# Kernel tuning notes

Hardware: AMD Instinct MI355X
Metric: run time of the kernel (lower is better)

Reference implementation:

```python
import jax, jax.numpy as jnp
import numpy as np

N_NODES = 50000
N_EDGES = 800000
D_IN = 1024
D_OUT = 256
LEAKY_SLOPE = 0.01  # F.leaky_relu default


def setup_inputs() -> dict:
    key = jax.random.key(0)
    k_x, k_w, k_b, k_src, k_dst, k_ew, k_norm = jax.random.split(key, 7)
    x = jax.random.normal(k_x, (N_NODES, D_IN), dtype=jnp.float32)
    # xavier_uniform-style scale for the weight
    limit = np.sqrt(6.0 / (D_IN + D_OUT)).astype(np.float32)
    weight = jax.random.uniform(k_w, (D_IN, D_OUT), dtype=jnp.float32, minval=-limit, maxval=limit)
    stdv = 1.0 / np.sqrt(D_OUT)
    bias = jax.random.uniform(k_b, (D_OUT,), dtype=jnp.float32, minval=-stdv, maxval=stdv)
    src = jax.random.randint(k_src, (N_EDGES,), 0, N_NODES, dtype=jnp.int64)
    dst = jax.random.randint(k_dst, (N_EDGES,), 0, N_NODES, dtype=jnp.int64)
    edge_index = jnp.stack([src, dst], axis=0)  # [2, E]
    edge_weight = jax.random.uniform(k_ew, (N_EDGES,), dtype=jnp.float32)
    norm = jax.random.uniform(k_norm, (N_NODES, 1), dtype=jnp.float32) + 0.5  # avoid div-by-~0
    return {"x": x, "weight": weight, "bias": bias, "edge_index": edge_index,
            "edge_weight": edge_weight, "norm": norm}


def reference(x, weight, bias, edge_index, edge_weight, norm):
    # support = input @ W            [N, D_OUT]
    support = x @ weight
    src = edge_index[0]
    dst = edge_index[1]
    # spmm(adj, support): out[i] = sum_{e: dst_e == i} w_e * support[src_e]
    msgs = support[src] * edge_weight[:, None]            # [E, D_OUT]
    out = jax.ops.segment_sum(msgs, dst, num_segments=x.shape[0])  # [N, D_OUT]
    out = out / norm + bias
    return jax.nn.leaky_relu(out, negative_slope=LEAKY_SLOPE)
```

## Files before the change

### kernel.cpp

```cpp
#include <hip/hip_runtime.h>
#include <hip/hip_bf16.h>

#define N_NODES 50000
#define N_EDGES 800000
#define D_IN    1024
#define D_OUT   256
#define CAP     64
#define LEAKY   0.01f

typedef __attribute__((ext_vector_type(8))) short bf16x8;
typedef __attribute__((ext_vector_type(4))) float f32x4;
typedef __attribute__((ext_vector_type(4))) int   i32x4;
typedef unsigned short u16;

__device__ __forceinline__ u16 f2bfu(float f) {
  uint32_t x = __float_as_uint(f);
  uint32_t r = (x + 0x7FFFu + ((x >> 16) & 1u)) >> 16;
  return (u16)r;
}
__device__ __forceinline__ float bfu2f(u16 u) {
  return __uint_as_float(((uint32_t)u) << 16);
}
__device__ __forceinline__ int swz2(int b) { return b ^ (((b >> 11) & 7) << 4); }

__global__ __launch_bounds__(256) void wconv_kernel(const float* __restrict__ w,
                                                    char* __restrict__ img,
                                                    int* __restrict__ deg) {
  const int t = blockIdx.x * 256 + threadIdx.x;
  if (t < N_NODES) deg[t] = 0;
  const int t2z = t + 32768;
  if (t2z < N_NODES) deg[t2z] = 0;

  const int s   = t >> 13;
  const int r13 = t & 8191;
  const int tt  = r13 >> 8;
  const int rem = r13 & 255;
  const int i   = rem >> 6;
  const int ln  = rem & 63;
  const int n   = s * 64 + i * 16 + (ln & 15);
  const int k0  = tt * 32 + (ln >> 4) * 8;
  bf16x8 v;
#pragma unroll
  for (int j = 0; j < 8; ++j) v[j] = (short)f2bfu(w[(size_t)(k0 + j) * D_OUT + n]);
  *(bf16x8*)(img + (size_t)t * 16) = v;
}

#define BM 64
#define GEMM_BLOCKS ((N_NODES + BM - 1) / BM)
#define BUILD_BLOCKS 64

__global__ __launch_bounds__(512) void gemm_build_kernel(
    const float* __restrict__ x, const char* __restrict__ img,
    u16* __restrict__ support,
    const int* __restrict__ ei, const float* __restrict__ ew,
    int* __restrict__ deg, int2* __restrict__ csr) {
  __shared__ char Xlds[BM * 2048];

  if (blockIdx.x < BUILD_BLOCKS) {
    const int t0 = blockIdx.x * 512 + threadIdx.x;
    for (int e = t0; e < N_EDGES; e += BUILD_BLOCKS * 512) {
      const int src = ei[e];
      const int dst = ei[N_EDGES + e];
      const float w = ew[e];
      const int slot = atomicAdd(&deg[dst], 1);
      if (slot < CAP) csr[dst * CAP + slot] = make_int2(src, __float_as_int(w));
    }
    return;
  }

  const int tid  = threadIdx.x;
  const int lane = tid & 63;
  const int wid  = tid >> 6;
  const int wn   = wid & 3;
  const int wm   = wid >> 2;
  const int l15  = lane & 15;
  const int l16  = lane >> 4;
  const int m0   = (blockIdx.x - BUILD_BLOCKS) * BM;

  {
    const int row  = tid >> 3;
    const int col8 = (tid & 7) * 8;
    const int xr   = min(m0 + row, N_NODES - 1);
    const float* xp = x + (size_t)xr * D_IN + col8;
#pragma unroll
    for (int c = 0; c < 16; ++c) {
      const f32x4 a = __builtin_nontemporal_load((const f32x4*)(xp + c * 64));
      const f32x4 b = __builtin_nontemporal_load((const f32x4*)(xp + c * 64 + 4));
      bf16x8 v;
      v[0] = (short)f2bfu(a[0]); v[1] = (short)f2bfu(a[1]);
      v[2] = (short)f2bfu(a[2]); v[3] = (short)f2bfu(a[3]);
      v[4] = (short)f2bfu(b[0]); v[5] = (short)f2bfu(b[1]);
      v[6] = (short)f2bfu(b[2]); v[7] = (short)f2bfu(b[3]);
      *(bf16x8*)(Xlds + swz2(row * 2048 + c * 128 + col8 * 2)) = v;
    }
  }
  __syncthreads();

  f32x4 acc[4][2];
#pragma unroll
  for (int i = 0; i < 4; ++i)
#pragma unroll
    for (int j = 0; j < 2; ++j) acc[i][j] = (f32x4)0.0f;

  const char* wp = img + (size_t)wn * 131072 + lane * 16;
  int xoff[2];
#pragma unroll
  for (int j = 0; j < 2; ++j)
    xoff[j] = (wm * 32 + j * 16 + l15) * 2048 + l16 * 16;

  bf16x8 afA[4], afB[4], bbA[2], bbB[2];
#pragma unroll
  for (int i = 0; i < 4; ++i) afA[i] = *(const bf16x8*)(wp + i * 1024);
#pragma unroll
  for (int j = 0; j < 2; ++j) bbA[j] = *(const bf16x8*)(Xlds + swz2(xoff[j]));

  for (int t = 0; t < 32; t += 2) {
#pragma unroll
    for (int i = 0; i < 4; ++i)
      afB[i] = *(const bf16x8*)(wp + (t + 1) * 4096 + i * 1024);
#pragma unroll
    for (int j = 0; j < 2; ++j)
      bbB[j] = *(const bf16x8*)(Xlds + swz2(xoff[j] + (t + 1) * 64));
#pragma unroll
    for (int i = 0; i < 4; ++i)
#pragma unroll
      for (int j = 0; j < 2; ++j)
        acc[i][j] = __builtin_amdgcn_mfma_f32_16x16x32_bf16(afA[i], bbA[j], acc[i][j], 0, 0, 0);
    if (t < 30) {
#pragma unroll
      for (int i = 0; i < 4; ++i)
        afA[i] = *(const bf16x8*)(wp + (t + 2) * 4096 + i * 1024);
#pragma unroll
      for (int j = 0; j < 2; ++j)
        bbA[j] = *(const bf16x8*)(Xlds + swz2(xoff[j] + (t + 2) * 64));
    }
#pragma unroll
    for (int i = 0; i < 4; ++i)
#pragma unroll
      for (int j = 0; j < 2; ++j)
        acc[i][j] = __builtin_amdgcn_mfma_f32_16x16x32_bf16(afB[i], bbB[j], acc[i][j], 0, 0, 0);
  }

#pragma unroll
  for (int j = 0; j < 2; ++j) {
    const int m = m0 + wm * 32 + j * 16 + l15;
    if (m < N_NODES) {
#pragma unroll
      for (int i = 0; i < 4; ++i) {
        const int n = wn * 64 + i * 16 + l16 * 4;
        ushort4 o;
        o.x = f2bfu(acc[i][j][0]);
        o.y = f2bfu(acc[i][j][1]);
        o.z = f2bfu(acc[i][j][2]);
        o.w = f2bfu(acc[i][j][3]);
        *(ushort4*)&support[(size_t)m * D_OUT + n] = o;
      }
    }
  }
}

__global__ __launch_bounds__(256) void agg_kernel(const u16* __restrict__ support,
                                                  const int* __restrict__ deg,
                                                  const int2* __restrict__ csr,
                                                  const float* __restrict__ norm,
                                                  const float* __restrict__ bias,
                                                  float* __restrict__ out) {
  const int lane = threadIdx.x & 63;
  const int wid  = threadIdx.x >> 6;
  const int node = blockIdx.x * 4 + wid;
  const int d    = min(deg[node], CAP);
  const int cb   = node * CAP;
  const int ch   = lane * 4;

  float a0 = 0.f, a1 = 0.f, a2 = 0.f, a3 = 0.f;
  int s = 0;

  for (; s + 16 <= d; s += 16) {
    i32x4 q[8];
#pragma unroll
    for (int i = 0; i < 8; ++i)
      q[i] = __builtin_nontemporal_load((const i32x4*)&csr[cb + s + 2 * i]);
    ushort4 v[16];
#pragma unroll
    for (int i = 0; i < 8; ++i) {
      v[2 * i]     = *(const ushort4*)&support[(size_t)q[i][0] * D_OUT + ch];
      v[2 * i + 1] = *(const ushort4*)&support[(size_t)q[i][2] * D_OUT + ch];
    }
#pragma unroll
    for (int i = 0; i < 8; ++i) {
      const float wa = __int_as_float(q[i][1]);
      const float wb = __int_as_float(q[i][3]);
      a0 = fmaf(wa, bfu2f(v[2 * i].x), a0);
      a1 = fmaf(wa, bfu2f(v[2 * i].y), a1);
      a2 = fmaf(wa, bfu2f(v[2 * i].z), a2);
      a3 = fmaf(wa, bfu2f(v[2 * i].w), a3);
      a0 = fmaf(wb, bfu2f(v[2 * i + 1].x), a0);
      a1 = fmaf(wb, bfu2f(v[2 * i + 1].y), a1);
      a2 = fmaf(wb, bfu2f(v[2 * i + 1].z), a2);
      a3 = fmaf(wb, bfu2f(v[2 * i + 1].w), a3);
    }
  }

  for (; s + 8 <= d; s += 8) {
    i32x4 q[4];
#pragma unroll
    for (int i = 0; i < 4; ++i)
      q[i] = __builtin_nontemporal_load((const i32x4*)&csr[cb + s + 2 * i]);
    ushort4 v[8];
#pragma unroll
    for (int i = 0; i < 4; ++i) {
      v[2 * i]     = *(const ushort4*)&support[(size_t)q[i][0] * D_OUT + ch];
      v[2 * i + 1] = *(const ushort4*)&support[(size_t)q[i][2] * D_OUT + ch];
    }
#pragma unroll
    for (int i = 0; i < 4; ++i) {
      const float wa = __int_as_float(q[i][1]);
      const float wb = __int_as_float(q[i][3]);
      a0 = fmaf(wa, bfu2f(v[2 * i].x), a0);
      a1 = fmaf(wa, bfu2f(v[2 * i].y), a1);
      a2 = fmaf(wa, bfu2f(v[2 * i].z), a2);
      a3 = fmaf(wa, bfu2f(v[2 * i].w), a3);
      a0 = fmaf(wb, bfu2f(v[2 * i + 1].x), a0);
      a1 = fmaf(wb, bfu2f(v[2 * i + 1].y), a1);
      a2 = fmaf(wb, bfu2f(v[2 * i + 1].z), a2);
      a3 = fmaf(wb, bfu2f(v[2 * i + 1].w), a3);
    }
  }

  for (; s < d; ++s) {
    const int2  e   = csr[cb + s];
    const float wgt = __int_as_float(e.y);
    const ushort4 v = *(const ushort4*)&support[(size_t)e.x * D_OUT + ch];
    a0 = fmaf(wgt, bfu2f(v.x), a0);
    a1 = fmaf(wgt, bfu2f(v.y), a1);
    a2 = fmaf(wgt, bfu2f(v.z), a2);
    a3 = fmaf(wgt, bfu2f(v.w), a3);
  }

  const float rn = 1.0f / norm[node];
  const float4 b = *(const float4*)&bias[ch];
  float o0 = fmaf(a0, rn, b.x);
  float o1 = fmaf(a1, rn, b.y);
  float o2 = fmaf(a2, rn, b.z);
  float o3 = fmaf(a3, rn, b.w);
  o0 = o0 > 0.f ? o0 : o0 * LEAKY;
  o1 = o1 > 0.f ? o1 : o1 * LEAKY;
  o2 = o2 > 0.f ? o2 : o2 * LEAKY;
  o3 = o3 > 0.f ? o3 : o3 * LEAKY;
  f32x4 ov;
  ov[0] = o0; ov[1] = o1; ov[2] = o2; ov[3] = o3;
  __builtin_nontemporal_store(ov, (f32x4*)&out[(size_t)node * D_OUT + ch]);
}

extern "C" void kernel_launch(void* const* d_in, const int* in_sizes, int n_in,
                              void* d_out, int out_size, void* d_ws, size_t ws_size,
                              hipStream_t stream) {
  const float* x    = (const float*)d_in[0];
  const float* w    = (const float*)d_in[1];
  const float* bias = (const float*)d_in[2];
  const int*   ei   = (const int*)d_in[3];
  const float* ew   = (const float*)d_in[4];
  const float* norm = (const float*)d_in[5];
  float* out = (float*)d_out;

  char* ws = (char*)d_ws;
  u16*   support = (u16*)  (ws);
  char*  img     =         (ws + 25600000);
  int2*  csr     = (int2*) (ws + 26124288);
  int*   deg     = (int*)  (ws + 51724288);

  wconv_kernel<<<128, 256, 0, stream>>>(w, img, deg);
  gemm_build_kernel<<<BUILD_BLOCKS + GEMM_BLOCKS, 512, 0, stream>>>(
      x, img, support, ei, ew, deg, csr);
  agg_kernel<<<N_NODES / 4, 256, 0, stream>>>(support, deg, csr, norm, bias, out);
}
```

Baseline: 183.0 us.

## Drop LDS staging; load x directly into registers with larger per-wave GEMM tiles

The GEMM no longer stages a converted 64-row x tile in shared memory. Each wave now loads fp32 x rows straight from global memory into registers, converts them to bf16 in-register, and computes a 64x128 output tile with double-buffered x fragments. The weight image is re-laid out to match, and blocks shrink to 256 threads covering two M-tiles. This removes the LDS footprint and the block-wide barrier to raise occupancy and overlap loads with MFMA, at the cost of much higher register pressure and less coalesced global x loads.

```diff
diff --git a/kernel.cpp b/kernel.cpp
--- a/kernel.cpp
+++ b/kernel.cpp
@@ -21,44 +21,39 @@
 __device__ __forceinline__ float bfu2f(u16 u) {
   return __uint_as_float(((uint32_t)u) << 16);
 }
-__device__ __forceinline__ int swz2(int b) { return b ^ (((b >> 11) & 7) << 4); }
 
 __global__ __launch_bounds__(256) void wconv_kernel(const float* __restrict__ w,
-                                                    char* __restrict__ img,
+                                                    char* __restrict__ wimg,
                                                     int* __restrict__ deg) {
-  const int t = blockIdx.x * 256 + threadIdx.x;
-  if (t < N_NODES) deg[t] = 0;
-  const int t2z = t + 32768;
-  if (t2z < N_NODES) deg[t2z] = 0;
-
-  const int s   = t >> 13;
-  const int r13 = t & 8191;
-  const int tt  = r13 >> 8;
-  const int rem = r13 & 255;
-  const int i   = rem >> 6;
-  const int ln  = rem & 63;
-  const int n   = s * 64 + i * 16 + (ln & 15);
-  const int k0  = tt * 32 + (ln >> 4) * 8;
+  const int u = blockIdx.x * 256 + threadIdx.x;
+  if (u < N_NODES) deg[u] = 0;
+  const int u2 = u + 32768;
+  if (u2 < N_NODES) deg[u2] = 0;
+
+  const int lane = u & 63;
+  const int nf   = (u >> 6) & 7;
+  const int wn   = (u >> 9) & 1;
+  const int t    = u >> 10;
+  const int n    = wn * 128 + nf * 16 + (lane & 15);
+  const int k0   = t * 32 + (lane >> 4) * 8;
   bf16x8 v;
 #pragma unroll
   for (int j = 0; j < 8; ++j) v[j] = (short)f2bfu(w[(size_t)(k0 + j) * D_OUT + n]);
-  *(bf16x8*)(img + (size_t)t * 16) = v;
-}
-
-#define BM 64
-#define GEMM_BLOCKS ((N_NODES + BM - 1) / BM)
-#define BUILD_BLOCKS 64
-
-__global__ __launch_bounds__(512) void gemm_build_kernel(
-    const float* __restrict__ x, const char* __restrict__ img,
+  *(bf16x8*)(wimg + (size_t)u * 16) = v;
+}
+
+#define MT_TILES ((N_NODES + 63) / 64)
+#define GEMM_BLOCKS ((MT_TILES + 1) / 2)
+#define BUILD_BLOCKS 60
+
+__global__ __launch_bounds__(256) void gemm_build_kernel(
+    const float* __restrict__ x, const char* __restrict__ wimg,
     u16* __restrict__ support,
     const int* __restrict__ ei, const float* __restrict__ ew,
     int* __restrict__ deg, int2* __restrict__ csr) {
-  __shared__ char Xlds[BM * 2048];
-
   if (blockIdx.x < BUILD_BLOCKS) {
-    const int t0 = blockIdx.x * 512 + threadIdx.x;
-    for (int e = t0; e < N_EDGES; e += BUILD_BLOCKS * 512) {
+    const int t0 = blockIdx.x * 256 + threadIdx.x;
+    for (int e = t0; e < N_EDGES; e += BUILD_BLOCKS * 256) {
       const int src = ei[e];
       const int dst = ei[N_EDGES + e];
       const float w = ew[e];
@@ -68,91 +63,88 @@
     return;
   }
 
+  const int bi   = blockIdx.x - BUILD_BLOCKS;
   const int tid  = threadIdx.x;
   const int lane = tid & 63;
   const int wid  = tid >> 6;
-  const int wn   = wid & 3;
-  const int wm   = wid >> 2;
+  const int mt   = bi * 2 + (wid >> 1);
+  const int wn   = wid & 1;
   const int l15  = lane & 15;
   const int l16  = lane >> 4;
-  const int m0   = (blockIdx.x - BUILD_BLOCKS) * BM;
-
-  {
-    const int row  = tid >> 3;
-    const int col8 = (tid & 7) * 8;
-    const int xr   = min(m0 + row, N_NODES - 1);
-    const float* xp = x + (size_t)xr * D_IN + col8;
-#pragma unroll
-    for (int c = 0; c < 16; ++c) {
-      const f32x4 a = __builtin_nontemporal_load((const f32x4*)(xp + c * 64));
-      const f32x4 b = __builtin_nontemporal_load((const f32x4*)(xp + c * 64 + 4));
-      bf16x8 v;
-      v[0] = (short)f2bfu(a[0]); v[1] = (short)f2bfu(a[1]);
-      v[2] = (short)f2bfu(a[2]); v[3] = (short)f2bfu(a[3]);
-      v[4] = (short)f2bfu(b[0]); v[5] = (short)f2bfu(b[1]);
-      v[6] = (short)f2bfu(b[2]); v[7] = (short)f2bfu(b[3]);
-      *(bf16x8*)(Xlds + swz2(row * 2048 + c * 128 + col8 * 2)) = v;
-    }
-  }
-  __syncthreads();
-
-  f32x4 acc[4][2];
-#pragma unroll
-  for (int i = 0; i < 4; ++i)
-#pragma unroll
-    for (int j = 0; j < 2; ++j) acc[i][j] = (f32x4)0.0f;
-
-  const char* wp = img + (size_t)wn * 131072 + lane * 16;
-  int xoff[2];
-#pragma unroll
-  for (int j = 0; j < 2; ++j)
-    xoff[j] = (wm * 32 + j * 16 + l15) * 2048 + l16 * 16;
-
-  bf16x8 afA[4], afB[4], bbA[2], bbB[2];
-#pragma unroll
-  for (int i = 0; i < 4; ++i) afA[i] = *(const bf16x8*)(wp + i * 1024);
-#pragma unroll
-  for (int j = 0; j < 2; ++j) bbA[j] = *(const bf16x8*)(Xlds + swz2(xoff[j]));
-
+
+  const float* xptr[4];
+#pragma unroll
+  for (int mf = 0; mf < 4; ++mf) {
+    int row = mt * 64 + mf * 16 + l15;
+    row = min(row, N_NODES - 1);
+    xptr[mf] = x + (size_t)row * D_IN + l16 * 8;
+  }
+  const char* wbase = wimg + wn * 8192 + (size_t)lane * 16;
+
+  f32x4 acc[8][4];
+#pragma unroll
+  for (int i = 0; i < 8; ++i)
+#pragma unroll
+    for (int j = 0; j < 4; ++j) acc[i][j] = (f32x4)0.0f;
+
+  f32x4 r0[4][2], r1[4][2];
+  bf16x8 wf[8];
+
+#define XFR(R, t) do {                                                     \
+    _Pragma("unroll")                                                      \
+    for (int mf_ = 0; mf_ < 4; ++mf_) {                                    \
+      R[mf_][0] = *(const f32x4*)(xptr[mf_] + (t) * 32);                   \
+      R[mf_][1] = *(const f32x4*)(xptr[mf_] + (t) * 32 + 4);               \
+    }                                                                      \
+  } while (0)
+
+#define WFL(t) do {                                                        \
+    _Pragma("unroll")                                                      \
+    for (int nf_ = 0; nf_ < 8; ++nf_)                                      \
+      wf[nf_] = *(const bf16x8*)(wbase + (size_t)(t) * 16384 + nf_ * 1024);\
+  } while (0)
+
+#define CVT_MFMA(R) do {                                                   \
+    _Pragma("unroll")                                                      \
+    for (int mf_ = 0; mf_ < 4; ++mf_) {                                    \
+      bf16x8 xb_;                                                          \
+      xb_[0] = (short)f2bfu(R[mf_][0][0]); xb_[1] = (short)f2bfu(R[mf_][0][1]); \
+      xb_[2] = (short)f2bfu(R[mf_][0][2]); xb_[3] = (short)f2bfu(R[mf_][0][3]); \
+      xb_[4] = (short)f2bfu(R[mf_][1][0]); xb_[5] = (short)f2bfu(R[mf_][1][1]); \
+      xb_[6] = (short)f2bfu(R[mf_][1][2]); xb_[7] = (short)f2bfu(R[mf_][1][3]); \
+      _Pragma("unroll")                                                    \
+      for (int nf_ = 0; nf_ < 8; ++nf_)                                    \
+        acc[nf_][mf_] = __builtin_amdgcn_mfma_f32_16x16x32_bf16(           \
+            wf[nf_], xb_, acc[nf_][mf_], 0, 0, 0);                         \
+    }                                                                      \
+  } while (0)
+
+  XFR(r0, 0);
   for (int t = 0; t < 32; t += 2) {
-#pragma unroll
-    for (int i = 0; i < 4; ++i)
-      afB[i] = *(const bf16x8*)(wp + (t + 1) * 4096 + i * 1024);
-#pragma unroll
-    for (int j = 0; j < 2; ++j)
-      bbB[j] = *(const bf16x8*)(Xlds + swz2(xoff[j] + (t + 1) * 64));
-#pragma unroll
-    for (int i = 0; i < 4; ++i)
-#pragma unroll
-      for (int j = 0; j < 2; ++j)
-        acc[i][j] = __builtin_amdgcn_mfma_f32_16x16x32_bf16(afA[i], bbA[j], acc[i][j], 0, 0, 0);
-    if (t < 30) {
-#pragma unroll
-      for (int i = 0; i < 4; ++i)
-        afA[i] = *(const bf16x8*)(wp + (t + 2) * 4096 + i * 1024);
-#pragma unroll
-      for (int j = 0; j < 2; ++j)
-        bbA[j] = *(const bf16x8*)(Xlds + swz2(xoff[j] + (t + 2) * 64));
-    }
-#pragma unroll
-    for (int i = 0; i < 4; ++i)
-#pragma unroll
-      for (int j = 0; j < 2; ++j)
-        acc[i][j] = __builtin_amdgcn_mfma_f32_16x16x32_bf16(afB[i], bbB[j], acc[i][j], 0, 0, 0);
-  }
-
-#pragma unroll
-  for (int j = 0; j < 2; ++j) {
-    const int m = m0 + wm * 32 + j * 16 + l15;
+    WFL(t);
+    XFR(r1, t + 1);
+    CVT_MFMA(r0);
+    WFL(t + 1);
+    XFR(r0, min(t + 2, 31));
+    CVT_MFMA(r1);
+  }
+
+#undef XFR
+#undef WFL
+#undef CVT_MFMA
+
+#pragma unroll
+  for (int mf = 0; mf < 4; ++mf) {
+    const int m = mt * 64 + mf * 16 + l15;
     if (m < N_NODES) {
 #pragma unroll
-      for (int i = 0; i < 4; ++i) {
-        const int n = wn * 64 + i * 16 + l16 * 4;
+      for (int nf = 0; nf < 8; ++nf) {
+        const int n = wn * 128 + nf * 16 + l16 * 4;
         ushort4 o;
-        o.x = f2bfu(acc[i][j][0]);
-        o.y = f2bfu(acc[i][j][1]);
-        o.z = f2bfu(acc[i][j][2]);
-        o.w = f2bfu(acc[i][j][3]);
+        o.x = f2bfu(acc[nf][mf][0]);
+        o.y = f2bfu(acc[nf][mf][1]);
+        o.z = f2bfu(acc[nf][mf][2]);
+        o.w = f2bfu(acc[nf][mf][3]);
         *(ushort4*)&support[(size_t)m * D_OUT + n] = o;
       }
     }
@@ -265,12 +257,12 @@
 
   char* ws = (char*)d_ws;
   u16*   support = (u16*)  (ws);
-  char*  img     =         (ws + 25600000);
+  char*  wimg    =         (ws + 25600000);
   int2*  csr     = (int2*) (ws + 26124288);
   int*   deg     = (int*)  (ws + 51724288);
 
-  wconv_kernel<<<128, 256, 0, stream>>>(w, img, deg);
-  gemm_build_kernel<<<BUILD_BLOCKS + GEMM_BLOCKS, 512, 0, stream>>>(
-      x, img, support, ei, ew, deg, csr);
+  wconv_kernel<<<128, 256, 0, stream>>>(w, wimg, deg);
+  gemm_build_kernel<<<BUILD_BLOCKS + GEMM_BLOCKS, 256, 0, stream>>>(
+      x, wimg, support, ei, ew, deg, csr);
   agg_kernel<<<N_NODES / 4, 256, 0, stream>>>(support, deg, csr, norm, bias, out);
 }
```

After: 195.6 us. 6.9% more time.
